# Optimization experiments

Hardware: AMD Instinct MI355X
Metric: run time of the kernel (lower is better)

Reference implementation:

```python
import jax, jax.numpy as jnp
import numpy as np

N_NODES = 2048
N_GRAPHS = 64
N_EDGES = 16384
B = 65536
META = 64
TX = 8
NOISE = 128
IN_DIM = N_NODES + 1 + 32 + TX  # 2089


def setup_inputs() -> dict:
    key = jax.random.key(0)
    ks = jax.random.split(key, 11)
    return {
        "batched_graphs": jax.random.randint(ks[0], (B,), 0, N_GRAPHS),
        "batched_chain": jax.random.normal(ks[1], (B,), dtype=jnp.float32),
        "trigger_data": jax.random.normal(ks[2], (B, META), dtype=jnp.float32),
        "tx_start_time": jax.random.normal(ks[3], (B, TX), dtype=jnp.float32),
        "edges": jax.random.randint(ks[4], (N_GRAPHS, 2, N_EDGES), 0, N_NODES),
        "gcn_w": jax.random.normal(ks[5], (), dtype=jnp.float32),
        "gcn_b": jax.random.normal(ks[6], (), dtype=jnp.float32) * 0.01,
        "trig_W": jax.random.normal(ks[7], (META, 32), dtype=jnp.float32) / np.sqrt(META),
        "trig_b": jnp.zeros((32,), dtype=jnp.float32),
        "emb_W": jax.random.normal(ks[8], (IN_DIM, NOISE), dtype=jnp.float32) / np.sqrt(IN_DIM),
        "emb_b": jnp.zeros((NOISE,), dtype=jnp.float32),
    }


def _gcn_one_graph(edge_index, w, b):
    # GCNConv(1,1) on x = ones(n_nodes,1): add self loops, sym-normalize.
    self_idx = jnp.arange(N_NODES, dtype=edge_index.dtype)
    src = jnp.concatenate([edge_index[0], self_idx])
    dst = jnp.concatenate([edge_index[1], self_idx])
    deg = jax.ops.segment_sum(jnp.ones(src.shape[0], jnp.float32), dst,
                              num_segments=N_NODES)
    dinv = jnp.where(deg > 0, jax.lax.rsqrt(deg), 0.0)
    norm = dinv[src] * dinv[dst]
    agg = jax.ops.segment_sum(norm, dst, num_segments=N_NODES)  # [n_nodes]
    return agg * w + b  # x @ W with x==1 is just w per node, plus bias


def reference(batched_graphs, batched_chain, trigger_data, tx_start_time,
              edges, gcn_w, gcn_b, trig_W, trig_b, emb_W, emb_b):
    # Per-graph GCN embeddings for all topologies (covers all uniques). [G, n_nodes]
    graph_emb = jax.vmap(lambda e: _gcn_one_graph(e, gcn_w, gcn_b))(edges)
    ge = graph_emb[batched_graphs]                         # [B, n_nodes] gather
    trig = jax.nn.relu(trigger_data @ trig_W + trig_b)     # [B, 32]
    x = jnp.concatenate(
        [ge, batched_chain[:, None], trig, tx_start_time], axis=1)  # [B, IN_DIM]
    return x @ emb_W + emb_b                               # [B, NOISE]
```

## Files before the change

### kernel.cpp

```cpp
#include <hip/hip_runtime.h>

#define NN 2048
#define NG 64
#define NE 16384
#define BB 65536
#define META 64
#define TXD 8
#define NOISE 128


__global__ __launch_bounds__(512) void gcn_kernel(
    const int* __restrict__ edges,
    const float* __restrict__ gcn_w,
    const float* __restrict__ gcn_b,
    const float* __restrict__ emb_W,
    float* __restrict__ graph_out)
{
    __shared__ int   s_cnt[NN];
    __shared__ float s_dinv[NN];
    __shared__ float s_val[NN];
    __shared__ float s_part[4][NOISE];
    const int g = blockIdx.x, tid = threadIdx.x;
    const int4* __restrict__ e4 = (const int4*)(edges + (size_t)g * 2 * NE);

    int4 ds[8];
    #pragma unroll
    for (int k = 0; k < 8; ++k) ds[k] = e4[4096 + k * 512 + tid];

    for (int n = tid; n < NN; n += 512) { s_cnt[n] = 1; s_val[n] = 0.0f; }
    __syncthreads();

    #pragma unroll
    for (int k = 0; k < 8; ++k) {
        atomicAdd(&s_cnt[ds[k].x], 1);
        atomicAdd(&s_cnt[ds[k].y], 1);
        atomicAdd(&s_cnt[ds[k].z], 1);
        atomicAdd(&s_cnt[ds[k].w], 1);
    }
    __syncthreads();
    for (int n = tid; n < NN; n += 512) s_dinv[n] = rsqrtf((float)s_cnt[n]);
    __syncthreads();

    #pragma unroll
    for (int k = 0; k < 8; ++k) {
        int4 sr = e4[k * 512 + tid];
        unsafeAtomicAdd(&s_val[ds[k].x], s_dinv[sr.x]);
        unsafeAtomicAdd(&s_val[ds[k].y], s_dinv[sr.y]);
        unsafeAtomicAdd(&s_val[ds[k].z], s_dinv[sr.z]);
        unsafeAtomicAdd(&s_val[ds[k].w], s_dinv[sr.w]);
    }
    __syncthreads();

    const float w = gcn_w[0], b = gcn_b[0];
    for (int n = tid; n < NN; n += 512) {
        float di = s_dinv[n];
        s_val[n] = di * (s_val[n] + di) * w + b;
    }
    __syncthreads();

    const int c = tid & 127, q = tid >> 7;
    const float* __restrict__ Wp = emb_W + (size_t)(q * 512) * NOISE + c;
    const float* __restrict__ ep = s_val + q * 512;
    float a0 = 0.f, a1 = 0.f, a2 = 0.f, a3 = 0.f;
    float a4 = 0.f, a5 = 0.f, a6 = 0.f, a7 = 0.f;
    #pragma unroll 2
    for (int i = 0; i < 512; i += 8) {
        a0 = fmaf(ep[i + 0], Wp[(i + 0) * NOISE], a0);
        a1 = fmaf(ep[i + 1], Wp[(i + 1) * NOISE], a1);
        a2 = fmaf(ep[i + 2], Wp[(i + 2) * NOISE], a2);
        a3 = fmaf(ep[i + 3], Wp[(i + 3) * NOISE], a3);
        a4 = fmaf(ep[i + 4], Wp[(i + 4) * NOISE], a4);
        a5 = fmaf(ep[i + 5], Wp[(i + 5) * NOISE], a5);
        a6 = fmaf(ep[i + 6], Wp[(i + 6) * NOISE], a6);
        a7 = fmaf(ep[i + 7], Wp[(i + 7) * NOISE], a7);
    }
    s_part[q][c] = ((a0 + a1) + (a2 + a3)) + ((a4 + a5) + (a6 + a7));
    __syncthreads();
    if (tid < NOISE)
        graph_out[g * NOISE + tid] = (s_part[0][tid] + s_part[1][tid])
                                   + (s_part[2][tid] + s_part[3][tid]);
}

#define ROWS 32
__global__ __launch_bounds__(256, 3) void main_kernel(
    const int* __restrict__ bg,
    const float* __restrict__ chain,
    const float* __restrict__ trig_in,
    const float* __restrict__ txs,
    const float* __restrict__ trig_W,
    const float* __restrict__ trig_b,
    const float* __restrict__ emb_W,
    const float* __restrict__ emb_b,
    const float* __restrict__ graph_out,
    float* __restrict__ out)
{
    __shared__ float s_td[ROWS * 68];
    __shared__ float s_twT[32 * 68];
    __shared__ float s_trig[ROWS * 36];
    __shared__ float s_tx[ROWS * TXD];
    __shared__ float s_ch[ROWS];
    __shared__ int   s_gi[ROWS];

    const int tid = threadIdx.x;
    const int row0 = blockIdx.x * ROWS;

    {
        const float4* __restrict__ gsrc =
            (const float4*)(trig_in + (size_t)row0 * META);
        #pragma unroll
        for (int k = 0; k < 2; ++k) {
            int t = tid + k * 256;
            int r = t >> 4, i4 = t & 15;
            *(float4*)&s_td[r * 68 + i4 * 4] = gsrc[t];
        }
    }
    {
        const float4* __restrict__ gsrc = (const float4*)trig_W;
        #pragma unroll
        for (int k = 0; k < 2; ++k) {
            int t = tid + k * 256;
            int i = t >> 3, j4 = (t & 7) * 4;
            float4 v = gsrc[t];
            s_twT[(j4 + 0) * 68 + i] = v.x;
            s_twT[(j4 + 1) * 68 + i] = v.y;
            s_twT[(j4 + 2) * 68 + i] = v.z;
            s_twT[(j4 + 3) * 68 + i] = v.w;
        }
    }
    if (tid < 64) {
        int r = tid >> 1, k4 = (tid & 1) * 4;
        *(float4*)&s_tx[r * TXD + k4] =
            ((const float4*)(txs + (size_t)row0 * TXD))[tid];
    } else if (tid < 96) {
        int r = tid - 64;
        s_ch[r] = chain[row0 + r];
    } else if (tid < 128) {
        int r = tid - 96;
        s_gi[r] = bg[row0 + r];
    }

    const int n0 = (tid & 63) * 2;
    float2 w2[32], w3[TXD];
    #pragma unroll
    for (int j = 0; j < 32; ++j)
        w2[j] = *(const float2*)&emb_W[(size_t)(2049 + j) * NOISE + n0];
    #pragma unroll
    for (int k = 0; k < TXD; ++k)
        w3[k] = *(const float2*)&emb_W[(size_t)(2081 + k) * NOISE + n0];
    const float2 w1   = *(const float2*)&emb_W[(size_t)2048 * NOISE + n0];
    const float2 bias = *(const float2*)&emb_b[n0];

    __syncthreads();

    {
        const int j0 = tid & 15;
        const int r0 = (tid >> 4) * 2;
        const float* __restrict__ tw0 = s_twT + j0 * 68;
        const float* __restrict__ tw1 = s_twT + (j0 + 16) * 68;
        const float* __restrict__ td0 = s_td + r0 * 68;
        const float* __restrict__ td1 = s_td + (r0 + 1) * 68;
        float b0 = trig_b[j0], b1 = trig_b[j0 + 16];
        float a00 = b0, a01 = b1, a10 = b0, a11 = b1;
        #pragma unroll
        for (int i = 0; i < META; i += 4) {
            float4 u0 = *(const float4*)(tw0 + i);
            float4 u1 = *(const float4*)(tw1 + i);
            float4 t0 = *(const float4*)(td0 + i);
            float4 t1 = *(const float4*)(td1 + i);
            a00 = fmaf(t0.x, u0.x, a00); a00 = fmaf(t0.y, u0.y, a00);
            a00 = fmaf(t0.z, u0.z, a00); a00 = fmaf(t0.w, u0.w, a00);
            a01 = fmaf(t0.x, u1.x, a01); a01 = fmaf(t0.y, u1.y, a01);
            a01 = fmaf(t0.z, u1.z, a01); a01 = fmaf(t0.w, u1.w, a01);
            a10 = fmaf(t1.x, u0.x, a10); a10 = fmaf(t1.y, u0.y, a10);
            a10 = fmaf(t1.z, u0.z, a10); a10 = fmaf(t1.w, u0.w, a10);
            a11 = fmaf(t1.x, u1.x, a11); a11 = fmaf(t1.y, u1.y, a11);
            a11 = fmaf(t1.z, u1.z, a11); a11 = fmaf(t1.w, u1.w, a11);
        }
        s_trig[r0 * 36 + j0]            = fmaxf(a00, 0.f);
        s_trig[r0 * 36 + j0 + 16]       = fmaxf(a01, 0.f);
        s_trig[(r0 + 1) * 36 + j0]      = fmaxf(a10, 0.f);
        s_trig[(r0 + 1) * 36 + j0 + 16] = fmaxf(a11, 0.f);
    }
    __syncthreads();

    const int wv = tid >> 6;
    int   gs[8];
    float chs[8];
    #pragma unroll
    for (int p = 0; p < 8; ++p) {
        const int r = p * 4 + wv;
        gs[p]  = s_gi[r];
        chs[p] = s_ch[r];
    }
    float2 go[8];
    #pragma unroll
    for (int p = 0; p < 8; ++p)
        go[p] = *(const float2*)&graph_out[gs[p] * NOISE + n0];

    #pragma unroll
    for (int p = 0; p < 8; ++p) {
        const int r = p * 4 + wv;
        const int row = row0 + r;
        float ax = bias.x + go[p].x + chs[p] * w1.x;
        float ay = bias.y + go[p].y + chs[p] * w1.y;
        const float4* __restrict__ tx4 = (const float4*)(s_tx + r * TXD);
        float4 t0 = tx4[0], t1 = tx4[1];
        ax = fmaf(t0.x, w3[0].x, ax); ay = fmaf(t0.x, w3[0].y, ay);
        ax = fmaf(t0.y, w3[1].x, ax); ay = fmaf(t0.y, w3[1].y, ay);
        ax = fmaf(t0.z, w3[2].x, ax); ay = fmaf(t0.z, w3[2].y, ay);
        ax = fmaf(t0.w, w3[3].x, ax); ay = fmaf(t0.w, w3[3].y, ay);
        ax = fmaf(t1.x, w3[4].x, ax); ay = fmaf(t1.x, w3[4].y, ay);
        ax = fmaf(t1.y, w3[5].x, ax); ay = fmaf(t1.y, w3[5].y, ay);
        ax = fmaf(t1.z, w3[6].x, ax); ay = fmaf(t1.z, w3[6].y, ay);
        ax = fmaf(t1.w, w3[7].x, ax); ay = fmaf(t1.w, w3[7].y, ay);
        const float* __restrict__ tg = s_trig + r * 36;
        #pragma unroll
        for (int q = 0; q < 8; ++q) {
            float4 t4 = *(const float4*)(tg + q * 4);
            ax = fmaf(t4.x, w2[4 * q + 0].x, ax); ay = fmaf(t4.x, w2[4 * q + 0].y, ay);
            ax = fmaf(t4.y, w2[4 * q + 1].x, ax); ay = fmaf(t4.y, w2[4 * q + 1].y, ay);
            ax = fmaf(t4.z, w2[4 * q + 2].x, ax); ay = fmaf(t4.z, w2[4 * q + 2].y, ay);
            ax = fmaf(t4.w, w2[4 * q + 3].x, ax); ay = fmaf(t4.w, w2[4 * q + 3].y, ay);
        }
        *(float2*)&out[(size_t)row * NOISE + n0] = make_float2(ax, ay);
    }
}

extern "C" void kernel_launch(void* const* d_in, const int* in_sizes, int n_in,
                              void* d_out, int out_size, void* d_ws, size_t ws_size,
                              hipStream_t stream) {
    const int*   bg      = (const int*)d_in[0];
    const float* chain   = (const float*)d_in[1];
    const float* trig_in = (const float*)d_in[2];
    const float* txs     = (const float*)d_in[3];
    const int*   edges   = (const int*)d_in[4];
    const float* gcn_w   = (const float*)d_in[5];
    const float* gcn_b   = (const float*)d_in[6];
    const float* trig_W  = (const float*)d_in[7];
    const float* trig_b  = (const float*)d_in[8];
    const float* emb_W   = (const float*)d_in[9];
    const float* emb_b   = (const float*)d_in[10];
    float* out = (float*)d_out;

    float* graph_out = (float*)d_ws;

    gcn_kernel<<<NG, 512, 0, stream>>>(edges, gcn_w, gcn_b, emb_W, graph_out);
    main_kernel<<<BB / ROWS, 256, 0, stream>>>(bg, chain, trig_in, txs, trig_W,
                                               trig_b, emb_W, emb_b, graph_out, out);
}
```

Baseline: 152.0 us.

## Split per-graph GCN across four blocks with cooperative grid syncs

```diff
diff --git a/kernel.cpp b/kernel.cpp
--- a/kernel.cpp
+++ b/kernel.cpp
@@ -1,4 +1,7 @@
 #include <hip/hip_runtime.h>
+#include <hip/hip_cooperative_groups.h>
+
+namespace cg = cooperative_groups;
 
 #define NN 2048
 #define NG 64
@@ -9,76 +12,109 @@
 #define NOISE 128
 
 
-__global__ __launch_bounds__(512) void gcn_kernel(
+__global__ __launch_bounds__(256) void gcn_coop_kernel(
     const int* __restrict__ edges,
     const float* __restrict__ gcn_w,
     const float* __restrict__ gcn_b,
     const float* __restrict__ emb_W,
-    float* __restrict__ graph_out)
+    float* __restrict__ graph_out,
+    int*   __restrict__ deg4,
+    float* __restrict__ acc4)
 {
     __shared__ int   s_cnt[NN];
     __shared__ float s_dinv[NN];
-    __shared__ float s_val[NN];
-    __shared__ float s_part[4][NOISE];
-    const int g = blockIdx.x, tid = threadIdx.x;
-    const int4* __restrict__ e4 = (const int4*)(edges + (size_t)g * 2 * NE);
-
-    int4 ds[8];
-    #pragma unroll
-    for (int k = 0; k < 8; ++k) ds[k] = e4[4096 + k * 512 + tid];
-
-    for (int n = tid; n < NN; n += 512) { s_cnt[n] = 1; s_val[n] = 0.0f; }
-    __syncthreads();
-
-    #pragma unroll
-    for (int k = 0; k < 8; ++k) {
+    __shared__ float s_emb[512];
+    __shared__ float s_part[NOISE];
+
+    const int b = blockIdx.x, g = b >> 2, q = b & 3, tid = threadIdx.x;
+    cg::grid_group grid = cg::this_grid();
+
+    if (q == 0 && tid < NOISE) graph_out[g * NOISE + tid] = 0.0f;
+
+    const int4* __restrict__ ed =
+        (const int4*)(edges + (size_t)g * 2 * NE + NE + q * 4096);
+    int4 ds[4];
+    #pragma unroll
+    for (int k = 0; k < 4; ++k) ds[k] = ed[k * 256 + tid];
+
+    for (int n = tid; n < NN; n += 256) s_cnt[n] = 0;
+    __syncthreads();
+    #pragma unroll
+    for (int k = 0; k < 4; ++k) {
         atomicAdd(&s_cnt[ds[k].x], 1);
         atomicAdd(&s_cnt[ds[k].y], 1);
         atomicAdd(&s_cnt[ds[k].z], 1);
         atomicAdd(&s_cnt[ds[k].w], 1);
     }
     __syncthreads();
-    for (int n = tid; n < NN; n += 512) s_dinv[n] = rsqrtf((float)s_cnt[n]);
-    __syncthreads();
-
-    #pragma unroll
-    for (int k = 0; k < 8; ++k) {
-        int4 sr = e4[k * 512 + tid];
-        unsafeAtomicAdd(&s_val[ds[k].x], s_dinv[sr.x]);
-        unsafeAtomicAdd(&s_val[ds[k].y], s_dinv[sr.y]);
-        unsafeAtomicAdd(&s_val[ds[k].z], s_dinv[sr.z]);
-        unsafeAtomicAdd(&s_val[ds[k].w], s_dinv[sr.w]);
-    }
-    __syncthreads();
-
-    const float w = gcn_w[0], b = gcn_b[0];
-    for (int n = tid; n < NN; n += 512) {
-        float di = s_dinv[n];
-        s_val[n] = di * (s_val[n] + di) * w + b;
-    }
-    __syncthreads();
-
-    const int c = tid & 127, q = tid >> 7;
-    const float* __restrict__ Wp = emb_W + (size_t)(q * 512) * NOISE + c;
-    const float* __restrict__ ep = s_val + q * 512;
-    float a0 = 0.f, a1 = 0.f, a2 = 0.f, a3 = 0.f;
-    float a4 = 0.f, a5 = 0.f, a6 = 0.f, a7 = 0.f;
-    #pragma unroll 2
-    for (int i = 0; i < 512; i += 8) {
-        a0 = fmaf(ep[i + 0], Wp[(i + 0) * NOISE], a0);
-        a1 = fmaf(ep[i + 1], Wp[(i + 1) * NOISE], a1);
-        a2 = fmaf(ep[i + 2], Wp[(i + 2) * NOISE], a2);
-        a3 = fmaf(ep[i + 3], Wp[(i + 3) * NOISE], a3);
-        a4 = fmaf(ep[i + 4], Wp[(i + 4) * NOISE], a4);
-        a5 = fmaf(ep[i + 5], Wp[(i + 5) * NOISE], a5);
-        a6 = fmaf(ep[i + 6], Wp[(i + 6) * NOISE], a6);
-        a7 = fmaf(ep[i + 7], Wp[(i + 7) * NOISE], a7);
-    }
-    s_part[q][c] = ((a0 + a1) + (a2 + a3)) + ((a4 + a5) + (a6 + a7));
-    __syncthreads();
-    if (tid < NOISE)
-        graph_out[g * NOISE + tid] = (s_part[0][tid] + s_part[1][tid])
-                                   + (s_part[2][tid] + s_part[3][tid]);
+    {
+        int* dp = deg4 + ((size_t)g * 4 + q) * NN;
+        for (int n = tid; n < NN; n += 256) dp[n] = s_cnt[n];
+    }
+    grid.sync();
+
+    {
+        const int* d0 = deg4 + (size_t)g * 4 * NN;
+        for (int n = tid; n < NN; n += 256) {
+            int d = d0[n] + d0[NN + n] + d0[2 * NN + n] + d0[3 * NN + n] + 1;
+            s_dinv[n] = rsqrtf((float)d);
+        }
+    }
+    float* s_val = (float*)s_cnt;
+    for (int n = tid; n < NN; n += 256) s_val[n] = 0.0f;
+    __syncthreads();
+    {
+        const int4* __restrict__ es =
+            (const int4*)(edges + (size_t)g * 2 * NE + q * 4096);
+        #pragma unroll
+        for (int k = 0; k < 4; ++k) {
+            int4 sr = es[k * 256 + tid];
+            unsafeAtomicAdd(&s_val[ds[k].x], s_dinv[sr.x]);
+            unsafeAtomicAdd(&s_val[ds[k].y], s_dinv[sr.y]);
+            unsafeAtomicAdd(&s_val[ds[k].z], s_dinv[sr.z]);
+            unsafeAtomicAdd(&s_val[ds[k].w], s_dinv[sr.w]);
+        }
+    }
+    __syncthreads();
+    {
+        float* ap = acc4 + ((size_t)g * 4 + q) * NN;
+        for (int n = tid; n < NN; n += 256) ap[n] = s_val[n];
+    }
+    grid.sync();
+
+    {
+        const float* a0 = acc4 + (size_t)g * 4 * NN + q * 512;
+        const float w = gcn_w[0], bb = gcn_b[0];
+        for (int n = tid; n < 512; n += 256) {
+            float sum = a0[n] + a0[NN + n] + a0[2 * NN + n] + a0[3 * NN + n];
+            float di = s_dinv[q * 512 + n];
+            s_emb[n] = di * (sum + di) * w + bb;
+        }
+    }
+    __syncthreads();
+    {
+        const int c = tid & 127, h = tid >> 7;
+        const float* __restrict__ Wp =
+            emb_W + (size_t)(q * 512 + h * 256) * NOISE + c;
+        const float* __restrict__ ep = s_emb + h * 256;
+        float a0 = 0.f, a1 = 0.f, a2 = 0.f, a3 = 0.f;
+        float a4 = 0.f, a5 = 0.f, a6 = 0.f, a7 = 0.f;
+        #pragma unroll 2
+        for (int i = 0; i < 256; i += 8) {
+            a0 = fmaf(ep[i + 0], Wp[(i + 0) * NOISE], a0);
+            a1 = fmaf(ep[i + 1], Wp[(i + 1) * NOISE], a1);
+            a2 = fmaf(ep[i + 2], Wp[(i + 2) * NOISE], a2);
+            a3 = fmaf(ep[i + 3], Wp[(i + 3) * NOISE], a3);
+            a4 = fmaf(ep[i + 4], Wp[(i + 4) * NOISE], a4);
+            a5 = fmaf(ep[i + 5], Wp[(i + 5) * NOISE], a5);
+            a6 = fmaf(ep[i + 6], Wp[(i + 6) * NOISE], a6);
+            a7 = fmaf(ep[i + 7], Wp[(i + 7) * NOISE], a7);
+        }
+        float acc_ = ((a0 + a1) + (a2 + a3)) + ((a4 + a5) + (a6 + a7));
+        if (h == 1) s_part[c] = acc_;
+        __syncthreads();
+        if (h == 0) unsafeAtomicAdd(&graph_out[g * NOISE + c], acc_ + s_part[c]);
+    }
 }
 
 #define ROWS 32
@@ -242,9 +278,17 @@
     const float* emb_b   = (const float*)d_in[10];
     float* out = (float*)d_out;
 
-    float* graph_out = (float*)d_ws;
-
-    gcn_kernel<<<NG, 512, 0, stream>>>(edges, gcn_w, gcn_b, emb_W, graph_out);
+    float* wsf       = (float*)d_ws;
+    float* graph_out = wsf;
+    int*   deg4      = (int*)(wsf + 8192);
+    float* acc4      = wsf + 8192 + 524288;
+
+    void* kargs[] = {
+        (void*)&edges, (void*)&gcn_w, (void*)&gcn_b, (void*)&emb_W,
+        (void*)&graph_out, (void*)&deg4, (void*)&acc4
+    };
+    hipLaunchCooperativeKernel(reinterpret_cast<void*>(gcn_coop_kernel),
+                               dim3(NG * 4), dim3(256), kargs, 0, stream);
     main_kernel<<<BB / ROWS, 256, 0, stream>>>(bg, chain, trig_in, txs, trig_W,
                                                trig_b, emb_W, emb_b, graph_out, out);
 }
```

New measurement: 211.2 us. 1.39x slower.
